# Optimization experiments

Measured on AMD Instinct MI355X. Metric: run time of the kernel, lower is better.

## Reference

```python
import jax, jax.numpy as jnp
import numpy as np

EPS = 1e-5
LEAK = 0.1
N_NODES = 100000
N_EDGES = 2000000
N_NF = 16
N_EF = 19
DIMS = [N_NF * 2 + N_EF, 64, 64, 32, 16, 8, 2]


def setup_inputs() -> dict:
    key = jax.random.key(0)
    ks = jax.random.split(key, 20)
    inp = {
        'x': jax.random.normal(ks[0], (N_NODES, N_NF), dtype=jnp.float32),
        'e': jax.random.normal(ks[1], (N_EDGES, N_EF), dtype=jnp.float32),
        'edge_index': jax.random.randint(ks[2], (2, N_EDGES), 0, N_NODES, dtype=jnp.int64),
        'xbatch': jnp.zeros((N_NODES,), dtype=jnp.int64),
        'bn_node_g': jnp.ones((N_NF,), jnp.float32),
        'bn_node_b': jnp.zeros((N_NF,), jnp.float32),
        'bn_edge_g': jnp.ones((N_EF,), jnp.float32),
        'bn_edge_b': jnp.zeros((N_EF,), jnp.float32),
    }
    # MLP weights: Lin(51,64), Lin(64,64), Lin(64,32), Lin(32,16), Lin(16,8), Lin(8,2)
    for i in range(6):
        fan_in, fan_out = DIMS[i], DIMS[i + 1]
        bound = 1.0 / np.sqrt(fan_in)
        inp[f'W{i+1}'] = jax.random.uniform(ks[4 + 2 * i], (fan_in, fan_out), jnp.float32, -bound, bound)
        inp[f'b{i+1}'] = jax.random.uniform(ks[5 + 2 * i], (fan_out,), jnp.float32, -bound, bound)
    return inp


def _batchnorm(v, g, b):
    # training-mode BatchNorm1d: biased batch statistics
    m = jnp.mean(v, axis=0)
    var = jnp.mean(jnp.square(v - m), axis=0)
    return (v - m) * (g / jnp.sqrt(var + EPS)) + b


def _lrelu(v):
    return jnp.where(v >= 0, v, LEAK * v)


def reference(x, e, edge_index, xbatch, bn_node_g, bn_node_b, bn_edge_g, bn_edge_b,
              W1, b1, W2, b2, W3, b3, W4, b4, W5, b5, W6, b6):
    e = _batchnorm(e, bn_edge_g, bn_edge_b)
    x = _batchnorm(x, bn_node_g, bn_node_b)
    src = x[edge_index[0]]  # [E, n_nf]
    dst = x[edge_index[1]]  # [E, n_nf]
    h = jnp.concatenate([src, dst, e], axis=1)  # [E, 2*n_nf + n_ef]
    h = _lrelu(h @ W1 + b1)
    h = _lrelu(h @ W2 + b2)
    h = _lrelu(h @ W3 + b3)
    h = _lrelu(h @ W4 + b4)
    h = _lrelu(h @ W5 + b5)
    edge_pred = h @ W6 + b6  # [E, 2]
    return edge_pred
```

## Files before the change

### kernel.cpp

```cpp
#include <hip/hip_runtime.h>

#define LEAK 0.1f
#define BN_EPS 1e-5f

constexpr int N_NODES = 100000;
constexpr int N_EDGES = 2000000;
constexpr int N_NF = 16;
constexpr int N_EF = 19;
constexpr int D0 = 2 * N_NF + N_EF;
constexpr int D1 = 64, D2 = 64, D3 = 32, D4 = 16, D5 = 8, D6 = 2;

constexpr int OFF_E_SUM = 0;
constexpr int OFF_E_SQ  = 32;
constexpr int OFF_X_SUM = 64;
constexpr int OFF_X_SQ  = 96;
constexpr int OFF_W1P   = 256;
constexpr int OFF_B1P   = OFF_W1P + D0 * D1;

typedef __attribute__((ext_vector_type(8))) short short8;
typedef __attribute__((ext_vector_type(4))) short short4v;
typedef __attribute__((ext_vector_type(4))) float f32x4;

static __device__ __forceinline__ short f2bf(float f) {
  unsigned u = __builtin_bit_cast(unsigned, f);
  unsigned r = (u + 0x7FFFu + ((u >> 16) & 1u)) >> 16;
  return (short)r;
}

template <int NF>
__global__ void col_stats_kernel(const float* __restrict__ v, int nrows,
                                 float* __restrict__ acc_sum,
                                 float* __restrict__ acc_sq) {
  float s[NF], qq[NF];
#pragma unroll
  for (int k = 0; k < NF; k++) { s[k] = 0.f; qq[k] = 0.f; }
  int tid = blockIdx.x * blockDim.x + threadIdx.x;
  int stride = gridDim.x * blockDim.x;
  for (int r = tid; r < nrows; r += stride) {
    const float* __restrict__ row = v + (size_t)r * NF;
#pragma unroll
    for (int k = 0; k < NF; k++) { float t = row[k]; s[k] += t; qq[k] += t * t; }
  }
#pragma unroll
  for (int k = 0; k < NF; k++) {
#pragma unroll
    for (int off = 32; off > 0; off >>= 1) {
      s[k] += __shfl_down(s[k], off);
      qq[k] += __shfl_down(qq[k], off);
    }
  }
  __shared__ float ls[4][2 * NF];
  int wave = threadIdx.x >> 6;
  int lane = threadIdx.x & 63;
  if (lane == 0) {
#pragma unroll
    for (int k = 0; k < NF; k++) { ls[wave][k] = s[k]; ls[wave][NF + k] = qq[k]; }
  }
  __syncthreads();
  if (threadIdx.x < 2 * NF) {
    float t = ls[0][threadIdx.x] + ls[1][threadIdx.x] + ls[2][threadIdx.x] +
              ls[3][threadIdx.x];
    if (threadIdx.x < NF) atomicAdd(&acc_sum[threadIdx.x], t);
    else                  atomicAdd(&acc_sq[threadIdx.x - NF], t);
  }
}

__global__ void fold_bn_kernel(const float* __restrict__ ws,
                               const float* __restrict__ ng, const float* __restrict__ nb,
                               const float* __restrict__ eg, const float* __restrict__ eb,
                               const float* __restrict__ W1, const float* __restrict__ b1,
                               float* __restrict__ W1p, float* __restrict__ b1p) {
  __shared__ float sc[D0], sh[D0];
  int t = threadIdx.x;
  if (t < D0) {
    float mean, var, g, b;
    if (t < 2 * N_NF) {
      int k = t & (N_NF - 1);
      mean = ws[OFF_X_SUM + k] / (float)N_NODES;
      var  = ws[OFF_X_SQ + k] / (float)N_NODES - mean * mean;
      g = ng[k]; b = nb[k];
    } else {
      int k = t - 2 * N_NF;
      mean = ws[OFF_E_SUM + k] / (float)N_EDGES;
      var  = ws[OFF_E_SQ + k] / (float)N_EDGES - mean * mean;
      g = eg[k]; b = eb[k];
    }
    float scale = g / sqrtf(var + BN_EPS);
    sc[t] = scale;
    sh[t] = b - mean * scale;
  }
  __syncthreads();
  if (t < D1) {
    float accb = b1[t];
    for (int i = 0; i < D0; i++) {
      float w = W1[i * D1 + t];
      W1p[i * D1 + t] = w * sc[i];
      accb += sh[i] * w;
    }
    b1p[t] = accb;
  }
}


__device__ __forceinline__ short8 load_wfrag(const float* __restrict__ W, int ldn,
                                             int kbase, int nbase, int kmax, int nmax,
                                             int q, int g) {
  short8 f;
#pragma unroll
  for (int j = 0; j < 8; j++) {
    int k = kbase + g * 8 + j;
    int n = nbase + q;
    float w = (k < kmax && n < nmax) ? W[k * ldn + n] : 0.f;
    f[j] = f2bf(w);
  }
  return f;
}

template <int KT, int NT>
__device__ __forceinline__ void mfma_layer(char* lb, int q, int g, int swzq,
                                           const short8 (&wf)[KT][NT],
                                           const float (&bv)[NT]) {
  short8 a[KT];
#pragma unroll
  for (int kk = 0; kk < KT; kk++)
    a[kk] = *(const short8*)(lb + q * 128 + ((kk * 64 + g * 16) ^ swzq));
  f32x4 acc[NT];
#pragma unroll
  for (int nt = 0; nt < NT; nt++) {
    acc[nt] = (f32x4){bv[nt], bv[nt], bv[nt], bv[nt]};
#pragma unroll
    for (int kk = 0; kk < KT; kk++)
      acc[nt] = __builtin_amdgcn_mfma_f32_16x16x32_bf16(a[kk], wf[kk][nt], acc[nt], 0, 0, 0);
  }
#pragma unroll
  for (int nt = 0; nt < NT; nt++) {
#pragma unroll
    for (int r = 0; r < 4; r++) {
      float v = acc[nt][r];
      v = fmaxf(v, LEAK * v);
      int mw = 4 * g + r;
      *(short*)(lb + mw * 128 + ((nt * 32 + q * 2) ^ ((mw & 7) << 4))) = f2bf(v);
    }
  }
}

#define RED16(v)                 \
  v += __shfl_xor(v, 1);         \
  v += __shfl_xor(v, 2);         \
  v += __shfl_xor(v, 4);         \
  v += __shfl_xor(v, 8);

__global__ __launch_bounds__(256) void edge_mlp_mfma_kernel(
    const float* __restrict__ x, const float* __restrict__ e,
    const int* __restrict__ ei,
    const float* __restrict__ W1p, const float* __restrict__ b1p,
    const float* __restrict__ W2, const float* __restrict__ b2,
    const float* __restrict__ W3, const float* __restrict__ b3,
    const float* __restrict__ W4, const float* __restrict__ b4,
    const float* __restrict__ W5, const float* __restrict__ b5,
    const float* __restrict__ W6, const float* __restrict__ b6,
    float* __restrict__ out) {
  __shared__ __align__(16) char actbuf[4 * 16 * 128];

  const int lane = threadIdx.x & 63;
  const int wave = threadIdx.x >> 6;
  const int q = lane & 15;
  const int g = lane >> 4;
  const int swzq = (q & 7) << 4;
  char* lb = actbuf + wave * 2048;

  short8 w1f[2][4], w2f[2][4], w3f[2][2], w4f[1][1];
  float b1v[4], b2v[4], b3v[2], b4v[1];
#pragma unroll
  for (int kk = 0; kk < 2; kk++)
#pragma unroll
    for (int nt = 0; nt < 4; nt++) {
      w1f[kk][nt] = load_wfrag(W1p, 64, kk * 32, nt * 16, D0, 64, q, g);
      w2f[kk][nt] = load_wfrag(W2, 64, kk * 32, nt * 16, 64, 64, q, g);
    }
#pragma unroll
  for (int kk = 0; kk < 2; kk++)
#pragma unroll
    for (int nt = 0; nt < 2; nt++)
      w3f[kk][nt] = load_wfrag(W3, 32, kk * 32, nt * 16, 64, 32, q, g);
  w4f[0][0] = load_wfrag(W4, 16, 0, 0, 32, 16, q, g);
  short8 w5f = load_wfrag(W5, 8, 0, 0, 16, 8, q, g);
#pragma unroll
  for (int nt = 0; nt < 4; nt++) { b1v[nt] = b1p[nt * 16 + q]; b2v[nt] = b2[nt * 16 + q]; }
#pragma unroll
  for (int nt = 0; nt < 2; nt++) b3v[nt] = b3[nt * 16 + q];
  b4v[0] = b4[q];
  float b5v = (q < 8) ? b5[q] : 0.f;
  float w60 = (q < 8) ? W6[q * 2 + 0] : 0.f;
  float w61 = (q < 8) ? W6[q * 2 + 1] : 0.f;
  float b60 = b6[0], b61 = b6[1];

  const int n_bt = N_EDGES / 64;
  for (int bt = blockIdx.x; bt < n_bt; bt += gridDim.x) {
    const int Eb = bt * 64 + wave * 16;
    const int eidx = Eb + q;

    const int src = ei[eidx];
    const int dst = ei[N_EDGES + eidx];
    {
      float4 vs = ((const float4*)x)[(size_t)src * 4 + g];
      short4v ps = {f2bf(vs.x), f2bf(vs.y), f2bf(vs.z), f2bf(vs.w)};
      *(short4v*)(lb + q * 128 + ((g * 8) ^ swzq)) = ps;
      float4 vd = ((const float4*)x)[(size_t)dst * 4 + g];
      short4v pd = {f2bf(vd.x), f2bf(vd.y), f2bf(vd.z), f2bf(vd.w)};
      *(short4v*)(lb + q * 128 + ((32 + g * 8) ^ swzq)) = pd;
      const float* er = e + (size_t)eidx * N_EF;
      float e0 = er[g * 4 + 0], e1 = er[g * 4 + 1], e2 = er[g * 4 + 2], e3 = er[g * 4 + 3];
      short4v pe = {f2bf(e0), f2bf(e1), f2bf(e2), f2bf(e3)};
      *(short4v*)(lb + q * 128 + ((64 + g * 8) ^ swzq)) = pe;
      short4v pt;
      if (g == 0) pt = (short4v){f2bf(er[16]), f2bf(er[17]), f2bf(er[18]), 0};
      else        pt = (short4v){0, 0, 0, 0};
      *(short4v*)(lb + q * 128 + ((96 + g * 8) ^ swzq)) = pt;
    }

    mfma_layer<2, 4>(lb, q, g, swzq, w1f, b1v);
    mfma_layer<2, 4>(lb, q, g, swzq, w2f, b2v);
    mfma_layer<2, 2>(lb, q, g, swzq, w3f, b3v);
    mfma_layer<1, 1>(lb, q, g, swzq, w4f, b4v);

    short8 a5 = *(const short8*)(lb + q * 128 + ((g * 16) ^ swzq));
    f32x4 acc5 = (f32x4){b5v, b5v, b5v, b5v};
    acc5 = __builtin_amdgcn_mfma_f32_16x16x32_bf16(a5, w5f, acc5, 0, 0, 0);
    float a50 = fmaxf(acc5[0], LEAK * acc5[0]);
    float a51 = fmaxf(acc5[1], LEAK * acc5[1]);
    float a52 = fmaxf(acc5[2], LEAK * acc5[2]);
    float a53 = fmaxf(acc5[3], LEAK * acc5[3]);

    float s00 = a50 * w60, s10 = a50 * w61;
    float s01 = a51 * w60, s11 = a51 * w61;
    float s02 = a52 * w60, s12 = a52 * w61;
    float s03 = a53 * w60, s13 = a53 * w61;
    RED16(s00) RED16(s10) RED16(s01) RED16(s11)
    RED16(s02) RED16(s12) RED16(s03) RED16(s13)
    if (q < 4) {
      float o0 = (q == 0) ? s00 : (q == 1) ? s01 : (q == 2) ? s02 : s03;
      float o1 = (q == 0) ? s10 : (q == 1) ? s11 : (q == 2) ? s12 : s13;
      ((float2*)out)[(size_t)Eb + g * 4 + q] = make_float2(o0 + b60, o1 + b61);
    }
  }
}

extern "C" void kernel_launch(void* const* d_in, const int* in_sizes, int n_in,
                              void* d_out, int out_size, void* d_ws, size_t ws_size,
                              hipStream_t stream) {
  const float* x  = (const float*)d_in[0];
  const float* e  = (const float*)d_in[1];
  const int*   ei = (const int*)d_in[2];
  const float* ng = (const float*)d_in[4];
  const float* nb = (const float*)d_in[5];
  const float* eg = (const float*)d_in[6];
  const float* eb = (const float*)d_in[7];
  const float* W1 = (const float*)d_in[8];
  const float* b1 = (const float*)d_in[9];
  const float* W2 = (const float*)d_in[10];
  const float* b2 = (const float*)d_in[11];
  const float* W3 = (const float*)d_in[12];
  const float* b3 = (const float*)d_in[13];
  const float* W4 = (const float*)d_in[14];
  const float* b4 = (const float*)d_in[15];
  const float* W5 = (const float*)d_in[16];
  const float* b5 = (const float*)d_in[17];
  const float* W6 = (const float*)d_in[18];
  const float* b6 = (const float*)d_in[19];
  float* out = (float*)d_out;
  float* ws  = (float*)d_ws;

  (void)hipMemsetAsync(ws, 0, 128 * sizeof(float), stream);

  col_stats_kernel<N_EF><<<1024, 256, 0, stream>>>(e, N_EDGES, ws + OFF_E_SUM, ws + OFF_E_SQ);
  col_stats_kernel<N_NF><<<128, 256, 0, stream>>>(x, N_NODES, ws + OFF_X_SUM, ws + OFF_X_SQ);
  fold_bn_kernel<<<1, 64, 0, stream>>>(ws, ng, nb, eg, eb, W1, b1,
                                       ws + OFF_W1P, ws + OFF_B1P);

  edge_mlp_mfma_kernel<<<2048, 256, 0, stream>>>(
      x, e, ei, ws + OFF_W1P, ws + OFF_B1P,
      W2, b2, W3, b3, W4, b4, W5, b5, W6, b6, out);
}
```

Baseline: 603.6 us.

## Prefetch next edge tile in registers, process two 16-row tiles per wave, coalesce edge stats

The edge MLP kernel now processes 32 edges per wave per iteration as two interleaved 16-row MFMA tiles. It software-prefetches the next iteration's index, node and edge-feature loads into registers while the current tile computes, which is meant to hide gather latency. The edge-feature statistics kernel is replaced by one that stages 256-row chunks into shared memory with coalesced float4 loads before reducing each column, instead of strided per-thread row reads. The costs are higher register pressure (launch bounds now ask for 2 blocks per CU) and more LDS per block.

```diff
diff --git a/kernel.cpp b/kernel.cpp
--- a/kernel.cpp
+++ b/kernel.cpp
@@ -25,6 +25,44 @@
   unsigned u = __builtin_bit_cast(unsigned, f);
   unsigned r = (u + 0x7FFFu + ((u >> 16) & 1u)) >> 16;
   return (short)r;
+}
+
+constexpr int SROWS = 256;
+__global__ __launch_bounds__(256) void e_stats_kernel(const float* __restrict__ v,
+                                                      float* __restrict__ acc_sum,
+                                                      float* __restrict__ acc_sq) {
+  __shared__ float lbuf[SROWS * N_EF];
+  const int t = threadIdx.x;
+  float s = 0.f, qq = 0.f;
+  const int col = t % N_EF;
+  const int rep = t / N_EF;
+  const int nchunks = (N_EDGES + SROWS - 1) / SROWS;
+  for (int c = blockIdx.x; c < nchunks; c += gridDim.x) {
+    const int nr = min(SROWS, N_EDGES - c * SROWS);
+    const int nf4 = nr * N_EF / 4;
+    const float4* src = (const float4*)(v + (size_t)c * SROWS * N_EF);
+    for (int i = t; i < nf4; i += 256) ((float4*)lbuf)[i] = src[i];
+    __syncthreads();
+    if (rep < 13) {
+      for (int r = rep; r < nr; r += 13) {
+        float x = lbuf[r * N_EF + col];
+        s += x; qq += x * x;
+      }
+    }
+    __syncthreads();
+  }
+  lbuf[t] = s; lbuf[256 + t] = qq;
+  __syncthreads();
+  if (t < N_EF) {
+    float ts = 0.f, tq = 0.f;
+#pragma unroll
+    for (int rp = 0; rp < 13; rp++) {
+      ts += lbuf[t + N_EF * rp];
+      tq += lbuf[256 + t + N_EF * rp];
+    }
+    atomicAdd(&acc_sum[t], ts);
+    atomicAdd(&acc_sq[t], tq);
+  }
 }
 
 template <int NF>
@@ -116,30 +154,75 @@
   return f;
 }
 
+struct Pref {
+  float4 vs, vd;
+  float e0, e1, e2, e3;
+  float t0, t1, t2;
+};
+
+__device__ __forceinline__ Pref load_gather(int eidx, int g,
+                                            const float* __restrict__ x,
+                                            const float* __restrict__ e,
+                                            const int* __restrict__ ei) {
+  Pref p;
+  const int src = ei[eidx];
+  const int dst = ei[N_EDGES + eidx];
+  p.vs = ((const float4*)x)[(size_t)src * 4 + g];
+  p.vd = ((const float4*)x)[(size_t)dst * 4 + g];
+  const float* er = e + (size_t)eidx * N_EF;
+  p.e0 = er[g * 4 + 0]; p.e1 = er[g * 4 + 1];
+  p.e2 = er[g * 4 + 2]; p.e3 = er[g * 4 + 3];
+  if (g == 0) { p.t0 = er[16]; p.t1 = er[17]; p.t2 = er[18]; }
+  else        { p.t0 = 0.f; p.t1 = 0.f; p.t2 = 0.f; }
+  return p;
+}
+
+__device__ __forceinline__ void stage_row(char* lb, int row, int swzq, int g,
+                                          const Pref& p) {
+  char* base = lb + row * 128;
+  short4v ps = {f2bf(p.vs.x), f2bf(p.vs.y), f2bf(p.vs.z), f2bf(p.vs.w)};
+  *(short4v*)(base + ((g * 8) ^ swzq)) = ps;
+  short4v pd = {f2bf(p.vd.x), f2bf(p.vd.y), f2bf(p.vd.z), f2bf(p.vd.w)};
+  *(short4v*)(base + ((32 + g * 8) ^ swzq)) = pd;
+  short4v pe = {f2bf(p.e0), f2bf(p.e1), f2bf(p.e2), f2bf(p.e3)};
+  *(short4v*)(base + ((64 + g * 8) ^ swzq)) = pe;
+  short4v pt = {f2bf(p.t0), f2bf(p.t1), f2bf(p.t2), 0};
+  *(short4v*)(base + ((96 + g * 8) ^ swzq)) = pt;
+}
+
 template <int KT, int NT>
-__device__ __forceinline__ void mfma_layer(char* lb, int q, int g, int swzq,
-                                           const short8 (&wf)[KT][NT],
-                                           const float (&bv)[NT]) {
-  short8 a[KT];
-#pragma unroll
-  for (int kk = 0; kk < KT; kk++)
-    a[kk] = *(const short8*)(lb + q * 128 + ((kk * 64 + g * 16) ^ swzq));
-  f32x4 acc[NT];
+__device__ __forceinline__ void mfma_layer2(char* lb, int q, int g, int swzq,
+                                            const short8 (&wf)[KT][NT],
+                                            const float (&bv)[NT]) {
+  short8 a0[KT], a1[KT];
+#pragma unroll
+  for (int kk = 0; kk < KT; kk++) {
+    a0[kk] = *(const short8*)(lb + q * 128 + ((kk * 64 + g * 16) ^ swzq));
+    a1[kk] = *(const short8*)(lb + (q + 16) * 128 + ((kk * 64 + g * 16) ^ swzq));
+  }
+  f32x4 acc0[NT], acc1[NT];
 #pragma unroll
   for (int nt = 0; nt < NT; nt++) {
-    acc[nt] = (f32x4){bv[nt], bv[nt], bv[nt], bv[nt]};
-#pragma unroll
-    for (int kk = 0; kk < KT; kk++)
-      acc[nt] = __builtin_amdgcn_mfma_f32_16x16x32_bf16(a[kk], wf[kk][nt], acc[nt], 0, 0, 0);
+    acc0[nt] = (f32x4){bv[nt], bv[nt], bv[nt], bv[nt]};
+    acc1[nt] = acc0[nt];
+#pragma unroll
+    for (int kk = 0; kk < KT; kk++) {
+      acc0[nt] = __builtin_amdgcn_mfma_f32_16x16x32_bf16(a0[kk], wf[kk][nt], acc0[nt], 0, 0, 0);
+      acc1[nt] = __builtin_amdgcn_mfma_f32_16x16x32_bf16(a1[kk], wf[kk][nt], acc1[nt], 0, 0, 0);
+    }
   }
 #pragma unroll
   for (int nt = 0; nt < NT; nt++) {
 #pragma unroll
     for (int r = 0; r < 4; r++) {
-      float v = acc[nt][r];
-      v = fmaxf(v, LEAK * v);
-      int mw = 4 * g + r;
-      *(short*)(lb + mw * 128 + ((nt * 32 + q * 2) ^ ((mw & 7) << 4))) = f2bf(v);
+      float v0 = acc0[nt][r];
+      v0 = fmaxf(v0, LEAK * v0);
+      int mw0 = 4 * g + r;
+      *(short*)(lb + mw0 * 128 + ((nt * 32 + q * 2) ^ ((mw0 & 7) << 4))) = f2bf(v0);
+      float v1 = acc1[nt][r];
+      v1 = fmaxf(v1, LEAK * v1);
+      int mw1 = 16 + 4 * g + r;
+      *(short*)(lb + mw1 * 128 + ((nt * 32 + q * 2) ^ ((mw1 & 7) << 4))) = f2bf(v1);
     }
   }
 }
@@ -150,7 +233,30 @@
   v += __shfl_xor(v, 4);         \
   v += __shfl_xor(v, 8);
 
-__global__ __launch_bounds__(256) void edge_mlp_mfma_kernel(
+__device__ __forceinline__ void tail56(char* lb, int roff, int q, int g, int swzq,
+                                       short8 w5f, float b5v, float w60, float w61,
+                                       float b60, float b61, float* out, int Eb) {
+  short8 a5 = *(const short8*)(lb + (q + roff) * 128 + ((g * 16) ^ swzq));
+  f32x4 acc5 = (f32x4){b5v, b5v, b5v, b5v};
+  acc5 = __builtin_amdgcn_mfma_f32_16x16x32_bf16(a5, w5f, acc5, 0, 0, 0);
+  float a50 = fmaxf(acc5[0], LEAK * acc5[0]);
+  float a51 = fmaxf(acc5[1], LEAK * acc5[1]);
+  float a52 = fmaxf(acc5[2], LEAK * acc5[2]);
+  float a53 = fmaxf(acc5[3], LEAK * acc5[3]);
+  float s00 = a50 * w60, s10 = a50 * w61;
+  float s01 = a51 * w60, s11 = a51 * w61;
+  float s02 = a52 * w60, s12 = a52 * w61;
+  float s03 = a53 * w60, s13 = a53 * w61;
+  RED16(s00) RED16(s10) RED16(s01) RED16(s11)
+  RED16(s02) RED16(s12) RED16(s03) RED16(s13)
+  if (q < 4) {
+    float o0 = (q == 0) ? s00 : (q == 1) ? s01 : (q == 2) ? s02 : s03;
+    float o1 = (q == 0) ? s10 : (q == 1) ? s11 : (q == 2) ? s12 : s13;
+    ((float2*)out)[(size_t)Eb + roff + g * 4 + q] = make_float2(o0 + b60, o1 + b61);
+  }
+}
+
+__global__ __launch_bounds__(256, 2) void edge_mlp_mfma_kernel(
     const float* __restrict__ x, const float* __restrict__ e,
     const int* __restrict__ ei,
     const float* __restrict__ W1p, const float* __restrict__ b1p,
@@ -160,14 +266,13 @@
     const float* __restrict__ W5, const float* __restrict__ b5,
     const float* __restrict__ W6, const float* __restrict__ b6,
     float* __restrict__ out) {
-  __shared__ __align__(16) char actbuf[4 * 16 * 128];
+  __shared__ __align__(16) char actbuf[4 * 2 * 32 * 128];
 
   const int lane = threadIdx.x & 63;
   const int wave = threadIdx.x >> 6;
   const int q = lane & 15;
   const int g = lane >> 4;
   const int swzq = (q & 7) << 4;
-  char* lb = actbuf + wave * 2048;
 
   short8 w1f[2][4], w2f[2][4], w3f[2][2], w4f[1][1];
   float b1v[4], b2v[4], b3v[2], b4v[1];
@@ -195,54 +300,34 @@
   float w61 = (q < 8) ? W6[q * 2 + 1] : 0.f;
   float b60 = b6[0], b61 = b6[1];
 
-  const int n_bt = N_EDGES / 64;
-  for (int bt = blockIdx.x; bt < n_bt; bt += gridDim.x) {
-    const int Eb = bt * 64 + wave * 16;
-    const int eidx = Eb + q;
-
-    const int src = ei[eidx];
-    const int dst = ei[N_EDGES + eidx];
-    {
-      float4 vs = ((const float4*)x)[(size_t)src * 4 + g];
-      short4v ps = {f2bf(vs.x), f2bf(vs.y), f2bf(vs.z), f2bf(vs.w)};
-      *(short4v*)(lb + q * 128 + ((g * 8) ^ swzq)) = ps;
-      float4 vd = ((const float4*)x)[(size_t)dst * 4 + g];
-      short4v pd = {f2bf(vd.x), f2bf(vd.y), f2bf(vd.z), f2bf(vd.w)};
-      *(short4v*)(lb + q * 128 + ((32 + g * 8) ^ swzq)) = pd;
-      const float* er = e + (size_t)eidx * N_EF;
-      float e0 = er[g * 4 + 0], e1 = er[g * 4 + 1], e2 = er[g * 4 + 2], e3 = er[g * 4 + 3];
-      short4v pe = {f2bf(e0), f2bf(e1), f2bf(e2), f2bf(e3)};
-      *(short4v*)(lb + q * 128 + ((64 + g * 8) ^ swzq)) = pe;
-      short4v pt;
-      if (g == 0) pt = (short4v){f2bf(er[16]), f2bf(er[17]), f2bf(er[18]), 0};
-      else        pt = (short4v){0, 0, 0, 0};
-      *(short4v*)(lb + q * 128 + ((96 + g * 8) ^ swzq)) = pt;
-    }
-
-    mfma_layer<2, 4>(lb, q, g, swzq, w1f, b1v);
-    mfma_layer<2, 4>(lb, q, g, swzq, w2f, b2v);
-    mfma_layer<2, 2>(lb, q, g, swzq, w3f, b3v);
-    mfma_layer<1, 1>(lb, q, g, swzq, w4f, b4v);
-
-    short8 a5 = *(const short8*)(lb + q * 128 + ((g * 16) ^ swzq));
-    f32x4 acc5 = (f32x4){b5v, b5v, b5v, b5v};
-    acc5 = __builtin_amdgcn_mfma_f32_16x16x32_bf16(a5, w5f, acc5, 0, 0, 0);
-    float a50 = fmaxf(acc5[0], LEAK * acc5[0]);
-    float a51 = fmaxf(acc5[1], LEAK * acc5[1]);
-    float a52 = fmaxf(acc5[2], LEAK * acc5[2]);
-    float a53 = fmaxf(acc5[3], LEAK * acc5[3]);
-
-    float s00 = a50 * w60, s10 = a50 * w61;
-    float s01 = a51 * w60, s11 = a51 * w61;
-    float s02 = a52 * w60, s12 = a52 * w61;
-    float s03 = a53 * w60, s13 = a53 * w61;
-    RED16(s00) RED16(s10) RED16(s01) RED16(s11)
-    RED16(s02) RED16(s12) RED16(s03) RED16(s13)
-    if (q < 4) {
-      float o0 = (q == 0) ? s00 : (q == 1) ? s01 : (q == 2) ? s02 : s03;
-      float o1 = (q == 0) ? s10 : (q == 1) ? s11 : (q == 2) ? s12 : s13;
-      ((float2*)out)[(size_t)Eb + g * 4 + q] = make_float2(o0 + b60, o1 + b61);
-    }
+  const int n_bt = N_EDGES / 128;
+  int buf = 0;
+  int bt0 = blockIdx.x;
+  Pref c1, c2;
+  if (bt0 < n_bt) {
+    const int Eb0 = bt0 * 128 + wave * 32;
+    c1 = load_gather(Eb0 + q, g, x, e, ei);
+    c2 = load_gather(Eb0 + 16 + q, g, x, e, ei);
+  }
+  for (int bt = bt0; bt < n_bt; bt += gridDim.x) {
+    const int Eb = bt * 128 + wave * 32;
+    const int nbt = bt + gridDim.x;
+    Pref n1 = c1, n2 = c2;
+    if (nbt < n_bt) {
+      const int nEb = nbt * 128 + wave * 32;
+      n1 = load_gather(nEb + q, g, x, e, ei);
+      n2 = load_gather(nEb + 16 + q, g, x, e, ei);
+    }
+    char* lb = actbuf + wave * 8192 + buf * 4096;
+    stage_row(lb, q, swzq, g, c1);
+    stage_row(lb, q + 16, swzq, g, c2);
+    mfma_layer2<2, 4>(lb, q, g, swzq, w1f, b1v);
+    mfma_layer2<2, 4>(lb, q, g, swzq, w2f, b2v);
+    mfma_layer2<2, 2>(lb, q, g, swzq, w3f, b3v);
+    mfma_layer2<1, 1>(lb, q, g, swzq, w4f, b4v);
+    tail56(lb, 0,  q, g, swzq, w5f, b5v, w60, w61, b60, b61, out, Eb);
+    tail56(lb, 16, q, g, swzq, w5f, b5v, w60, w61, b60, b61, out, Eb);
+    c1 = n1; c2 = n2; buf ^= 1;
   }
 }
 
@@ -273,7 +358,7 @@
 
   (void)hipMemsetAsync(ws, 0, 128 * sizeof(float), stream);
 
-  col_stats_kernel<N_EF><<<1024, 256, 0, stream>>>(e, N_EDGES, ws + OFF_E_SUM, ws + OFF_E_SQ);
+  e_stats_kernel<<<1024, 256, 0, stream>>>(e, ws + OFF_E_SUM, ws + OFF_E_SQ);
   col_stats_kernel<N_NF><<<128, 256, 0, stream>>>(x, N_NODES, ws + OFF_X_SUM, ws + OFF_X_SQ);
   fold_bn_kernel<<<1, 64, 0, stream>>>(ws, ng, nb, eg, eb, W1, b1,
                                        ws + OFF_W1P, ws + OFF_B1P);
```

New measurement: 531.4 us. 1.14x faster.
